# Kernel tuning notes

Hardware: AMD Instinct MI355X
Metric: run time of the kernel (lower is better)

## Reference

```python
import jax, jax.numpy as jnp
import numpy as np

DECAY = 0.1   # self.decay
EPS = 1e-5    # self.eps
NORM_EPS = 1e-8


def setup_inputs() -> dict:
    key = jax.random.key(0)
    k1, k2, k3 = jax.random.split(key, 3)
    N, D, K, H = 65536, 32, 4096, 1
    x = jax.random.normal(k1, (N, D), dtype=jnp.float32)
    embed = jax.random.normal(k2, (H, K, D), dtype=jnp.float32)
    cluster_size = jnp.zeros((H, K), dtype=jnp.float32)
    embed_avg = jax.random.normal(k3, (H, K, D), dtype=jnp.float32)
    return {"x": x, "embed": embed, "cluster_size": cluster_size, "embed_avg": embed_avg}


def reference(x, embed, cluster_size, embed_avg):
    H, K, D = embed.shape
    orig_shape = x.shape
    # needs_codebook_dim: x.ndim < 4 -> add codebook dim, flatten to [h, n, d]
    f = x.reshape(H, -1, D).astype(jnp.float32)
    # L2-normalize features and codebook (as in forward)
    fn = f / (jnp.linalg.norm(f, axis=-1, keepdims=True) + NORM_EPS)
    en = embed / (jnp.linalg.norm(embed, axis=-1, keepdims=True) + NORM_EPS)
    # negative pairwise squared euclidean distance: [h, n, K]
    f2 = jnp.sum(fn * fn, axis=-1)[..., None]          # [h, n, 1]
    e2 = jnp.sum(en * en, axis=-1)[:, None, :]          # [h, 1, K]
    dist = -(f2 - 2.0 * jnp.einsum('hnd,hkd->hnk', fn, en) + e2)
    # hard assignment (argmax of negative distance == nearest code)
    embed_ind = jnp.argmax(dist, axis=-1)               # [h, n] int
    onehot = jax.nn.one_hot(embed_ind, K, dtype=fn.dtype)  # [h, n, K]
    # batched_embedding: one-hot @ codebook
    quantize = jnp.einsum('hnk,hkd->hnd', onehot, en)
    # EMA codebook statistics (batched_bincount + scatter-add of features)
    bins = jnp.sum(onehot, axis=1)                       # [h, K]
    embed_sum = jnp.einsum('hnd,hnk->hkd', fn, onehot)   # [h, K, d]
    cluster_size_new = cluster_size * DECAY + bins * (1.0 - DECAY)
    embed_avg_new = embed_avg * DECAY + embed_sum * (1.0 - DECAY)
    # laplace-smoothed normalization of the EMA codebook
    n_total = jnp.sum(cluster_size_new, axis=-1, keepdims=True)
    smoothed = (cluster_size_new + EPS) / (n_total + K * EPS) * n_total
    embed_updated = embed_avg_new / smoothed[..., None]
    quantize = quantize.reshape(orig_shape)
    return quantize, embed_ind, cluster_size_new, embed_avg_new, embed_updated
```

## Files before the change

kernel.cpp:

```cpp
#include <hip/hip_runtime.h>
#include <float.h>

#define DECAY 0.1f
#define OMD   0.9f
#define EPS   1e-5f
#define NORM_EPS 1e-8f

static constexpr int D = 32;

typedef __attribute__((ext_vector_type(8))) short s16x8;
typedef __attribute__((ext_vector_type(4))) float f32x4_t;

__device__ __forceinline__ float bf2f(short s) {
    return __uint_as_float(((unsigned int)(unsigned short)s) << 16);
}

struct Split3 { short b0, b1, b2; };

__device__ __forceinline__ Split3 split3(float v) {
    const unsigned int u0 = __float_as_uint(v) & 0xFFFF0000u;
    const float r  = v - __uint_as_float(u0);
    const unsigned int u1 = __float_as_uint(r) & 0xFFFF0000u;
    const float r2 = r - __uint_as_float(u1);
    Split3 s;
    s.b0 = (short)(u0 >> 16);
    s.b1 = (short)(u1 >> 16);
    s.b2 = (short)(__float_as_uint(r2) >> 16);
    return s;
}

__global__ void prep_codebook(const float* __restrict__ embed,
                              unsigned short* __restrict__ bfrag,
                              int K) {
    const int k = blockIdx.x * blockDim.x + threadIdx.x;
    if (k >= K) return;
    float v[D]; float ssq = 0.f;
#pragma unroll
    for (int d = 0; d < D; ++d) { v[d] = embed[(size_t)k * D + d]; ssq += v[d] * v[d]; }
    const float inv = 1.0f / (sqrtf(ssq) + NORM_EPS);
    float e2 = 0.f;
    short p0[D], p1[D], p2[D];
#pragma unroll
    for (int d = 0; d < D; ++d) {
        const float e = v[d] * inv;
        e2 += e * e;
        const Split3 s = split3(2.0f * e);
        p0[d] = s.b0; p1[d] = s.b1; p2[d] = s.b2;
    }
    char* base = (char*)bfrag + (size_t)(k >> 4) * 3136;
    const int col = k & 15;
    *(float*)(base + 3072 + col * 4) = -e2;
#pragma unroll
    for (int g = 0; g < 4; ++g) {
        const int lid = g * 16 + col;
        s16x8 s0, s1, s2;
#pragma unroll
        for (int i = 0; i < 8; ++i) { s0[i] = p0[g*8+i]; s1[i] = p1[g*8+i]; s2[i] = p2[g*8+i]; }
        *(s16x8*)(base +    0 + lid * 16) = s0;
        *(s16x8*)(base + 1024 + lid * 16) = s1;
        *(s16x8*)(base + 2048 + lid * 16) = s2;
    }
}

struct Btile { s16x8 b0, b1, b2; float ne2; };

__global__ __launch_bounds__(512)
void assign_kernel(const float* __restrict__ x,
                   const unsigned short* __restrict__ bfrag,
                   float* __restrict__ out_quant,
                   float* __restrict__ out_ind,
                   float* __restrict__ bins,
                   float* __restrict__ esum,
                   int N, int K) {
    constexpr int PB = 32;
    __shared__ char  sm[6144];
    __shared__ float teamS[8][PB];
    __shared__ float teamC[8][PB];
    __shared__ int   best_c[PB];

    const int tid  = threadIdx.x;
    const int lane = tid & 63;
    const int team = tid >> 6;
    const int n0   = blockIdx.x * PB;
    const int col  = lane & 15;

    float fn_r[8];
    if (tid < 4 * PB) {
        const int p = tid >> 2, q = tid & 3;
        const float* xp = &x[(size_t)(n0 + p) * D + q * 8];
        const float4 va = *(const float4*)(xp);
        const float4 vb = *(const float4*)(xp + 4);
        float ssq = va.x*va.x + va.y*va.y + va.z*va.z + va.w*va.w
                  + vb.x*vb.x + vb.y*vb.y + vb.z*vb.z + vb.w*vb.w;
        ssq += __shfl_xor(ssq, 1);
        ssq += __shfl_xor(ssq, 2);
        const float inv = 1.0f / (sqrtf(ssq) + NORM_EPS);
        fn_r[0]=va.x*inv; fn_r[1]=va.y*inv; fn_r[2]=va.z*inv; fn_r[3]=va.w*inv;
        fn_r[4]=vb.x*inv; fn_r[5]=vb.y*inv; fn_r[6]=vb.z*inv; fn_r[7]=vb.w*inv;
        char* dst = &sm[(p >> 4) * 3072 + (q * 16 + (p & 15)) * 16];
        s16x8 s0, s1, s2;
#pragma unroll
        for (int i = 0; i < 8; ++i) {
            const Split3 s = split3(fn_r[i]);
            s0[i] = s.b0; s1[i] = s.b1; s2[i] = s.b2;
        }
        *(s16x8*)(dst) = s0; *(s16x8*)(dst + 1024) = s1; *(s16x8*)(dst + 2048) = s2;
    }
    __syncthreads();

    s16x8 A[2][3];
#pragma unroll
    for (int pg = 0; pg < 2; ++pg) {
#pragma unroll
        for (int pl = 0; pl < 3; ++pl)
            A[pg][pl] = *(const s16x8*)&sm[pg * 3072 + pl * 1024 + lane * 16];
    }

    float bestS[2][4], bestC[2][4];
#pragma unroll
    for (int pg = 0; pg < 2; ++pg)
#pragma unroll
        for (int r = 0; r < 4; ++r) { bestS[pg][r] = -1e30f; bestC[pg][r] = 0.f; }

    const int NT = K >> 4;
    const int HT = NT >> 3;
    const int t0 = team * HT;
    const char* gp  = (const char*)bfrag + (size_t)t0 * 3136 + lane * 16;
    const char* gpe = (const char*)bfrag + (size_t)t0 * 3136 + 3072 + (size_t)col * 4;

    auto compute = [&](const Btile& T, float codef) {
        const f32x4_t initX = {T.ne2, T.ne2, T.ne2, T.ne2};
#pragma unroll
        for (int pg = 0; pg < 2; ++pg) {
            f32x4_t X = __builtin_amdgcn_mfma_f32_16x16x32_bf16(A[pg][0], T.b0, initX, 0, 0, 0);
            X = __builtin_amdgcn_mfma_f32_16x16x32_bf16(A[pg][0], T.b1, X, 0, 0, 0);
            X = __builtin_amdgcn_mfma_f32_16x16x32_bf16(A[pg][1], T.b1, X, 0, 0, 0);
            X = __builtin_amdgcn_mfma_f32_16x16x32_bf16(A[pg][1], T.b0, X, 0, 0, 0);
            X = __builtin_amdgcn_mfma_f32_16x16x32_bf16(A[pg][0], T.b2, X, 0, 0, 0);
            X = __builtin_amdgcn_mfma_f32_16x16x32_bf16(A[pg][2], T.b0, X, 0, 0, 0);
            X = __builtin_amdgcn_mfma_f32_16x16x32_bf16(A[pg][1], T.b2, X, 0, 0, 0);
            X = __builtin_amdgcn_mfma_f32_16x16x32_bf16(A[pg][2], T.b1, X, 0, 0, 0);
#pragma unroll
            for (int r = 0; r < 4; ++r) {
                const float sc = X[r];
                if (sc > bestS[pg][r]) { bestS[pg][r] = sc; bestC[pg][r] = codef; }
            }
        }
    };

    auto loadB = [&](const char* base, const char* ebase, Btile& T) {
        T.b0  = *(const s16x8*)(base);
        T.b1  = *(const s16x8*)(base + 1024);
        T.b2  = *(const s16x8*)(base + 2048);
        T.ne2 = *(const float*)(ebase);
    };

    Btile U, V;
    loadB(gp,        gpe,        U);
    loadB(gp + 3136, gpe + 3136, V);

    float cb = (float)(t0 * 16 + col);
    for (int t = 0; t < HT; t += 2) {
        compute(U, cb);
        loadB(gp + 2 * 3136, gpe + 2 * 3136, U);
        compute(V, cb + 16.0f);
        loadB(gp + 3 * 3136, gpe + 3 * 3136, V);
        gp += 6272; gpe += 6272;
        cb += 32.0f;
    }

#pragma unroll
    for (int pg = 0; pg < 2; ++pg)
#pragma unroll
        for (int r = 0; r < 4; ++r) {
            float s = bestS[pg][r], c = bestC[pg][r];
#pragma unroll
            for (int off = 8; off >= 1; off >>= 1) {
                const float os = __shfl_xor(s, off);
                const float oc = __shfl_xor(c, off);
                if (os > s || (os == s && oc < c)) { s = os; c = oc; }
            }
            if (col == 0) {
                const int p = pg * 16 + (lane >> 4) * 4 + r;
                teamS[team][p] = s;
                teamC[team][p] = c;
            }
        }
    __syncthreads();

    if (tid < PB) {
        float s = teamS[0][tid];
        float c = teamC[0][tid];
#pragma unroll
        for (int t = 1; t < 8; ++t) {
            const float st = teamS[t][tid];
            const float ct = teamC[t][tid];
            if (st > s) { s = st; c = ct; }
        }
        out_ind[n0 + tid] = c;
        best_c[tid] = (int)c;
        atomicAdd(&bins[(int)c], 1.0f);
    }
    __syncthreads();

    if (tid < 4 * PB) {
        const int p = tid >> 2, q = tid & 3;
        const int b = best_c[p];
#pragma unroll
        for (int i = 0; i < 8; ++i)
            atomicAdd(&esum[(size_t)b * D + q * 8 + i], fn_r[i]);
        const char* bp = (const char*)bfrag + (size_t)(b >> 4) * 3136;
        const int lid = q * 16 + (b & 15);
        const s16x8 s0 = *(const s16x8*)(bp +    0 + lid * 16);
        const s16x8 s1 = *(const s16x8*)(bp + 1024 + lid * 16);
        const s16x8 s2 = *(const s16x8*)(bp + 2048 + lid * 16);
        float o[8];
#pragma unroll
        for (int i = 0; i < 8; ++i)
            o[i] = 0.5f * ((bf2f(s0[i]) + bf2f(s1[i])) + bf2f(s2[i]));
        float4 q0 = {o[0], o[1], o[2], o[3]};
        float4 q1 = {o[4], o[5], o[6], o[7]};
        *(float4*)&out_quant[(size_t)(n0 + p) * D + q * 8]     = q0;
        *(float4*)&out_quant[(size_t)(n0 + p) * D + q * 8 + 4] = q1;
    }
}

__global__ void reduce_kernel(const float* __restrict__ cluster_size,
                              const float* __restrict__ bins,
                              float* __restrict__ out_cs,
                              float* __restrict__ n_total, int K) {
    __shared__ float red[256];
    float s = 0.f;
    for (int k = threadIdx.x; k < K; k += 256) {
        const float v = cluster_size[k] * DECAY + bins[k] * OMD;
        out_cs[k] = v;
        s += v;
    }
    red[threadIdx.x] = s;
    __syncthreads();
    for (int off = 128; off > 0; off >>= 1) {
        if (threadIdx.x < off) red[threadIdx.x] += red[threadIdx.x + off];
        __syncthreads();
    }
    if (threadIdx.x == 0) n_total[0] = red[0];
}

__global__ void finalize_kernel(const float* __restrict__ embed_avg,
                                const float* __restrict__ esum,
                                const float* __restrict__ out_cs,
                                const float* __restrict__ n_total,
                                float* __restrict__ out_avg,
                                float* __restrict__ out_upd,
                                int K) {
    const int i = blockIdx.x * blockDim.x + threadIdx.x;
    if (i >= K * D) return;
    const int k = i >> 5;
    const float avg = embed_avg[i] * DECAY + esum[i] * OMD;
    out_avg[i] = avg;
    const float nt = n_total[0];
    const float cs = out_cs[k];
    const float sm = (cs + EPS) / (nt + (float)K * EPS) * nt;
    out_upd[i] = avg / sm;
}

extern "C" void kernel_launch(void* const* d_in, const int* in_sizes, int n_in,
                              void* d_out, int out_size, void* d_ws, size_t ws_size,
                              hipStream_t stream) {
    const float* x            = (const float*)d_in[0];
    const float* embed        = (const float*)d_in[1];
    const float* cluster_size = (const float*)d_in[2];
    const float* embed_avg    = (const float*)d_in[3];

    const int KD = in_sizes[1];
    const int K  = in_sizes[2];
    const int N  = in_sizes[0] / D;

    float* ws = (float*)d_ws;
    unsigned short* bfrag = (unsigned short*)ws;
    float* bins  = ws + (size_t)K * 49;
    float* esum  = bins + K;
    float* ntot  = esum + KD;

    float* out     = (float*)d_out;
    float* o_quant = out;
    float* o_ind   = o_quant + (size_t)N * D;
    float* o_cs    = o_ind   + N;
    float* o_avg   = o_cs    + K;
    float* o_upd   = o_avg   + KD;

    (void)hipMemsetAsync(bins, 0, (size_t)(K + KD + 1) * sizeof(float), stream);

    prep_codebook<<<(K + 63) / 64, 64, 0, stream>>>(embed, bfrag, K);
    assign_kernel<<<N / 32, 512, 0, stream>>>(x, bfrag,
                                              o_quant, o_ind, bins, esum, N, K);
    reduce_kernel<<<1, 256, 0, stream>>>(cluster_size, bins, o_cs, ntot, K);
    finalize_kernel<<<(KD + 255) / 256, 256, 0, stream>>>(embed_avg, esum, o_cs, ntot,
                                                          o_avg, o_upd, K);
}
```

Before: 142.6 us.

## Switch codebook distance GEMM to 32x32x16 bf16 MFMA tiles

Replaces the 16x16x32 MFMA path with 32x32x16 bf16 MFMAs, covering all 32 points of a block by 32 codes per instruction group. The codebook fragment layout in prep_codebook, the LDS A-fragment layout, the argmax lane reduction and the quantize lookup are all reorganised for the new tile shape. Normalized features now go through an LDS buffer instead of being held in registers. The aim is fewer MFMA issues and less argmax bookkeeping per code, in exchange for more registers per thread (16 accumulators, 16 running bests, six B fragments per tile), which may lower occupancy.

```diff
diff --git a/kernel.cpp b/kernel.cpp
--- a/kernel.cpp
+++ b/kernel.cpp
@@ -9,7 +9,7 @@
 static constexpr int D = 32;
 
 typedef __attribute__((ext_vector_type(8))) short s16x8;
-typedef __attribute__((ext_vector_type(4))) float f32x4_t;
+typedef __attribute__((ext_vector_type(16))) float f32x16_t;
 
 __device__ __forceinline__ float bf2f(short s) {
     return __uint_as_float(((unsigned int)(unsigned short)s) << 16);
@@ -47,22 +47,28 @@
         const Split3 s = split3(2.0f * e);
         p0[d] = s.b0; p1[d] = s.b1; p2[d] = s.b2;
     }
-    char* base = (char*)bfrag + (size_t)(k >> 4) * 3136;
-    const int col = k & 15;
-    *(float*)(base + 3072 + col * 4) = -e2;
-#pragma unroll
-    for (int g = 0; g < 4; ++g) {
-        const int lid = g * 16 + col;
-        s16x8 s0, s1, s2;
-#pragma unroll
-        for (int i = 0; i < 8; ++i) { s0[i] = p0[g*8+i]; s1[i] = p1[g*8+i]; s2[i] = p2[g*8+i]; }
-        *(s16x8*)(base +    0 + lid * 16) = s0;
-        *(s16x8*)(base + 1024 + lid * 16) = s1;
-        *(s16x8*)(base + 2048 + lid * 16) = s2;
-    }
-}
-
-struct Btile { s16x8 b0, b1, b2; float ne2; };
+    char* base = (char*)bfrag + (size_t)(k >> 5) * 6272;
+    const int col = k & 31;
+    *(float*)(base + 6144 + col * 4) = -e2;
+#pragma unroll
+    for (int c = 0; c < 2; ++c) {
+#pragma unroll
+        for (int hi = 0; hi < 2; ++hi) {
+            const int lane = hi * 32 + col;
+            s16x8 s0, s1, s2;
+#pragma unroll
+            for (int i = 0; i < 8; ++i) {
+                const int d = c * 16 + hi * 8 + i;
+                s0[i] = p0[d]; s1[i] = p1[d]; s2[i] = p2[d];
+            }
+            *(s16x8*)(base + (0 * 2 + c) * 1024 + lane * 16) = s0;
+            *(s16x8*)(base + (1 * 2 + c) * 1024 + lane * 16) = s1;
+            *(s16x8*)(base + (2 * 2 + c) * 1024 + lane * 16) = s2;
+        }
+    }
+}
+
+struct Btile { s16x8 b00, b01, b10, b11, b20, b21; float ne2; };
 
 __global__ __launch_bounds__(512)
 void assign_kernel(const float* __restrict__ x,
@@ -74,6 +80,7 @@
                    int N, int K) {
     constexpr int PB = 32;
     __shared__ char  sm[6144];
+    __shared__ float fnlds[PB][D];
     __shared__ float teamS[8][PB];
     __shared__ float teamC[8][PB];
     __shared__ int   best_c[PB];
@@ -82,9 +89,8 @@
     const int lane = tid & 63;
     const int team = tid >> 6;
     const int n0   = blockIdx.x * PB;
-    const int col  = lane & 15;
-
-    float fn_r[8];
+    const int col  = lane & 31;
+
     if (tid < 4 * PB) {
         const int p = tid >> 2, q = tid & 3;
         const float* xp = &x[(size_t)(n0 + p) * D + q * 8];
@@ -95,97 +101,100 @@
         ssq += __shfl_xor(ssq, 1);
         ssq += __shfl_xor(ssq, 2);
         const float inv = 1.0f / (sqrtf(ssq) + NORM_EPS);
-        fn_r[0]=va.x*inv; fn_r[1]=va.y*inv; fn_r[2]=va.z*inv; fn_r[3]=va.w*inv;
-        fn_r[4]=vb.x*inv; fn_r[5]=vb.y*inv; fn_r[6]=vb.z*inv; fn_r[7]=vb.w*inv;
-        char* dst = &sm[(p >> 4) * 3072 + (q * 16 + (p & 15)) * 16];
+        float fr[8];
+        fr[0]=va.x*inv; fr[1]=va.y*inv; fr[2]=va.z*inv; fr[3]=va.w*inv;
+        fr[4]=vb.x*inv; fr[5]=vb.y*inv; fr[6]=vb.z*inv; fr[7]=vb.w*inv;
+#pragma unroll
+        for (int i = 0; i < 8; ++i) fnlds[p][q * 8 + i] = fr[i];
+        const int c = q >> 1, hi = q & 1;
+        char* d0 = &sm[c * 1024 + (hi * 32 + p) * 16];
         s16x8 s0, s1, s2;
 #pragma unroll
         for (int i = 0; i < 8; ++i) {
-            const Split3 s = split3(fn_r[i]);
+            const Split3 s = split3(fr[i]);
             s0[i] = s.b0; s1[i] = s.b1; s2[i] = s.b2;
         }
-        *(s16x8*)(dst) = s0; *(s16x8*)(dst + 1024) = s1; *(s16x8*)(dst + 2048) = s2;
+        *(s16x8*)(d0) = s0; *(s16x8*)(d0 + 2048) = s1; *(s16x8*)(d0 + 4096) = s2;
     }
     __syncthreads();
 
-    s16x8 A[2][3];
-#pragma unroll
-    for (int pg = 0; pg < 2; ++pg) {
-#pragma unroll
-        for (int pl = 0; pl < 3; ++pl)
-            A[pg][pl] = *(const s16x8*)&sm[pg * 3072 + pl * 1024 + lane * 16];
-    }
-
-    float bestS[2][4], bestC[2][4];
-#pragma unroll
-    for (int pg = 0; pg < 2; ++pg)
-#pragma unroll
-        for (int r = 0; r < 4; ++r) { bestS[pg][r] = -1e30f; bestC[pg][r] = 0.f; }
-
-    const int NT = K >> 4;
-    const int HT = NT >> 3;
-    const int t0 = team * HT;
-    const char* gp  = (const char*)bfrag + (size_t)t0 * 3136 + lane * 16;
-    const char* gpe = (const char*)bfrag + (size_t)t0 * 3136 + 3072 + (size_t)col * 4;
+    s16x8 A00 = *(const s16x8*)&sm[0 * 2048 + 0 * 1024 + lane * 16];
+    s16x8 A01 = *(const s16x8*)&sm[0 * 2048 + 1 * 1024 + lane * 16];
+    s16x8 A10 = *(const s16x8*)&sm[1 * 2048 + 0 * 1024 + lane * 16];
+    s16x8 A11 = *(const s16x8*)&sm[1 * 2048 + 1 * 1024 + lane * 16];
+    s16x8 A20 = *(const s16x8*)&sm[2 * 2048 + 0 * 1024 + lane * 16];
+    s16x8 A21 = *(const s16x8*)&sm[2 * 2048 + 1 * 1024 + lane * 16];
+
+    float bestS[16], bestC[16];
+#pragma unroll
+    for (int r = 0; r < 16; ++r) { bestS[r] = -1e30f; bestC[r] = 0.f; }
+
+    const int NT32 = K >> 5;
+    const int HT   = NT32 >> 3;
+    const int t0   = team * HT;
+    const char* gp  = (const char*)bfrag + (size_t)t0 * 6272 + lane * 16;
+    const char* gpe = (const char*)bfrag + (size_t)t0 * 6272 + 6144 + (size_t)col * 4;
+
+#define MFMA32(Af, Bf, C) __builtin_amdgcn_mfma_f32_32x32x16_bf16(Af, Bf, C, 0, 0, 0)
 
     auto compute = [&](const Btile& T, float codef) {
-        const f32x4_t initX = {T.ne2, T.ne2, T.ne2, T.ne2};
-#pragma unroll
-        for (int pg = 0; pg < 2; ++pg) {
-            f32x4_t X = __builtin_amdgcn_mfma_f32_16x16x32_bf16(A[pg][0], T.b0, initX, 0, 0, 0);
-            X = __builtin_amdgcn_mfma_f32_16x16x32_bf16(A[pg][0], T.b1, X, 0, 0, 0);
-            X = __builtin_amdgcn_mfma_f32_16x16x32_bf16(A[pg][1], T.b1, X, 0, 0, 0);
-            X = __builtin_amdgcn_mfma_f32_16x16x32_bf16(A[pg][1], T.b0, X, 0, 0, 0);
-            X = __builtin_amdgcn_mfma_f32_16x16x32_bf16(A[pg][0], T.b2, X, 0, 0, 0);
-            X = __builtin_amdgcn_mfma_f32_16x16x32_bf16(A[pg][2], T.b0, X, 0, 0, 0);
-            X = __builtin_amdgcn_mfma_f32_16x16x32_bf16(A[pg][1], T.b2, X, 0, 0, 0);
-            X = __builtin_amdgcn_mfma_f32_16x16x32_bf16(A[pg][2], T.b1, X, 0, 0, 0);
-#pragma unroll
-            for (int r = 0; r < 4; ++r) {
-                const float sc = X[r];
-                if (sc > bestS[pg][r]) { bestS[pg][r] = sc; bestC[pg][r] = codef; }
-            }
+        f32x16_t X;
+#pragma unroll
+        for (int r = 0; r < 16; ++r) X[r] = T.ne2;
+        X = MFMA32(A00, T.b00, X); X = MFMA32(A01, T.b01, X);
+        X = MFMA32(A00, T.b10, X); X = MFMA32(A01, T.b11, X);
+        X = MFMA32(A10, T.b10, X); X = MFMA32(A11, T.b11, X);
+        X = MFMA32(A10, T.b00, X); X = MFMA32(A11, T.b01, X);
+        X = MFMA32(A00, T.b20, X); X = MFMA32(A01, T.b21, X);
+        X = MFMA32(A20, T.b00, X); X = MFMA32(A21, T.b01, X);
+        X = MFMA32(A10, T.b20, X); X = MFMA32(A11, T.b21, X);
+        X = MFMA32(A20, T.b10, X); X = MFMA32(A21, T.b11, X);
+#pragma unroll
+        for (int r = 0; r < 16; ++r) {
+            const float sc = X[r];
+            if (sc > bestS[r]) { bestS[r] = sc; bestC[r] = codef; }
         }
     };
 
     auto loadB = [&](const char* base, const char* ebase, Btile& T) {
-        T.b0  = *(const s16x8*)(base);
-        T.b1  = *(const s16x8*)(base + 1024);
-        T.b2  = *(const s16x8*)(base + 2048);
+        T.b00 = *(const s16x8*)(base);
+        T.b01 = *(const s16x8*)(base + 1024);
+        T.b10 = *(const s16x8*)(base + 2048);
+        T.b11 = *(const s16x8*)(base + 3072);
+        T.b20 = *(const s16x8*)(base + 4096);
+        T.b21 = *(const s16x8*)(base + 5120);
         T.ne2 = *(const float*)(ebase);
     };
 
     Btile U, V;
     loadB(gp,        gpe,        U);
-    loadB(gp + 3136, gpe + 3136, V);
-
-    float cb = (float)(t0 * 16 + col);
+    loadB(gp + 6272, gpe + 6272, V);
+
+    float cb = (float)(t0 * 32 + col);
     for (int t = 0; t < HT; t += 2) {
         compute(U, cb);
-        loadB(gp + 2 * 3136, gpe + 2 * 3136, U);
-        compute(V, cb + 16.0f);
-        loadB(gp + 3 * 3136, gpe + 3 * 3136, V);
-        gp += 6272; gpe += 6272;
-        cb += 32.0f;
-    }
-
-#pragma unroll
-    for (int pg = 0; pg < 2; ++pg)
-#pragma unroll
-        for (int r = 0; r < 4; ++r) {
-            float s = bestS[pg][r], c = bestC[pg][r];
-#pragma unroll
-            for (int off = 8; off >= 1; off >>= 1) {
-                const float os = __shfl_xor(s, off);
-                const float oc = __shfl_xor(c, off);
-                if (os > s || (os == s && oc < c)) { s = os; c = oc; }
-            }
-            if (col == 0) {
-                const int p = pg * 16 + (lane >> 4) * 4 + r;
-                teamS[team][p] = s;
-                teamC[team][p] = c;
-            }
-        }
+        loadB(gp + 2 * 6272, gpe + 2 * 6272, U);
+        compute(V, cb + 32.0f);
+        loadB(gp + 3 * 6272, gpe + 3 * 6272, V);
+        gp += 12544; gpe += 12544;
+        cb += 64.0f;
+    }
+
+#pragma unroll
+    for (int r = 0; r < 16; ++r) {
+        float s = bestS[r], c = bestC[r];
+#pragma unroll
+        for (int off = 16; off >= 1; off >>= 1) {
+            const float os = __shfl_xor(s, off);
+            const float oc = __shfl_xor(c, off);
+            if (os > s || (os == s && oc < c)) { s = os; c = oc; }
+        }
+        if (col == 0) {
+            const int p = (r & 3) + 8 * (r >> 2) + 4 * (lane >> 5);
+            teamS[team][p] = s;
+            teamC[team][p] = c;
+        }
+    }
     __syncthreads();
 
     if (tid < PB) {
@@ -208,12 +217,13 @@
         const int b = best_c[p];
 #pragma unroll
         for (int i = 0; i < 8; ++i)
-            atomicAdd(&esum[(size_t)b * D + q * 8 + i], fn_r[i]);
-        const char* bp = (const char*)bfrag + (size_t)(b >> 4) * 3136;
-        const int lid = q * 16 + (b & 15);
-        const s16x8 s0 = *(const s16x8*)(bp +    0 + lid * 16);
-        const s16x8 s1 = *(const s16x8*)(bp + 1024 + lid * 16);
-        const s16x8 s2 = *(const s16x8*)(bp + 2048 + lid * 16);
+            atomicAdd(&esum[(size_t)b * D + q * 8 + i], fnlds[p][q * 8 + i]);
+        const char* bp = (const char*)bfrag + (size_t)(b >> 5) * 6272;
+        const int c = q >> 1, hi = q & 1;
+        const int lsl = (hi * 32 + (b & 31)) * 16;
+        const s16x8 s0 = *(const s16x8*)(bp + (0 * 2 + c) * 1024 + lsl);
+        const s16x8 s1 = *(const s16x8*)(bp + (1 * 2 + c) * 1024 + lsl);
+        const s16x8 s2 = *(const s16x8*)(bp + (2 * 2 + c) * 1024 + lsl);
         float o[8];
 #pragma unroll
         for (int i = 0; i < 8; ++i)
```

Result: slower. 225.3 us (+58.0%).
